# Optimization experiments

Measured on AMD Instinct MI355X. Metric: run time of the kernel, lower is better.

The kernel has to match this reference:

```python
import jax, jax.numpy as jnp
import numpy as np

B, S, HID = 2, 2048, 4096
NH, NKV, HD = 32, 8, 128
SCALING = HD ** -0.5
Q_SIZE = NH * HD          # 4096
KV_SIZE = NKV * HD        # 1024
GROUPS = NH // NKV        # 4


def setup_inputs() -> dict:
    key = jax.random.key(0)
    ks = jax.random.split(key, 5)
    hidden_states = jax.random.normal(ks[0], (B, S, HID), dtype=jnp.float32)
    # Realistic rotary embeddings: cos/sin of position-dependent angles, HF layout [B, S, HD]
    inv_freq = 1.0 / (10000.0 ** (jnp.arange(0, HD, 2, dtype=jnp.float32) / HD))  # [HD/2]
    pos = jnp.arange(S, dtype=jnp.float32)
    freqs = pos[:, None] * inv_freq[None, :]                 # [S, HD/2]
    emb = jnp.concatenate([freqs, freqs], axis=-1)           # [S, HD]
    cos = jnp.broadcast_to(jnp.cos(emb), (B, S, HD))
    sin = jnp.broadcast_to(jnp.sin(emb), (B, S, HD))
    w_qkv = jax.random.normal(ks[1], (Q_SIZE + 2 * KV_SIZE, HID), dtype=jnp.float32) * (HID ** -0.5)
    w_o = jax.random.normal(ks[2], (HID, Q_SIZE), dtype=jnp.float32) * (Q_SIZE ** -0.5)
    return {"hidden_states": hidden_states, "cos": cos, "sin": sin, "w_qkv": w_qkv, "w_o": w_o}


def _rotate_half(x):
    x1, x2 = jnp.split(x, 2, axis=-1)
    return jnp.concatenate([-x2, x1], axis=-1)


def reference(hidden_states, cos, sin, w_qkv, w_o):
    b, s, _ = hidden_states.shape
    # Fused QKV projection (attention_bias=False for llama)
    qkv = jnp.einsum('bsh,oh->bso', hidden_states, w_qkv)    # [B, S, Q+2KV]
    q = qkv[..., :Q_SIZE].reshape(b, s, NH, HD).transpose(0, 2, 1, 3)                       # [B, NH, S, D]
    k = qkv[..., Q_SIZE:Q_SIZE + KV_SIZE].reshape(b, s, NKV, HD).transpose(0, 2, 1, 3)      # [B, NKV, S, D]
    v = qkv[..., Q_SIZE + KV_SIZE:].reshape(b, s, NKV, HD).transpose(0, 2, 1, 3)            # [B, NKV, S, D]
    # Rotary position embedding (HF apply_rotary_pos_emb, unsqueeze over heads)
    c = cos[:, None, :, :]
    sn = sin[:, None, :, :]
    q = q * c + _rotate_half(q) * sn
    k = k * c + _rotate_half(k) * sn
    # GQA: repeat KV heads across groups
    k = jnp.repeat(k, GROUPS, axis=1)   # [B, NH, S, D]
    v = jnp.repeat(v, GROUPS, axis=1)
    # Causal SDPA
    scores = jnp.einsum('bhqd,bhkd->bhqk', q, k) * SCALING
    causal = jnp.tril(jnp.ones((s, s), dtype=bool))
    scores = jnp.where(causal[None, None], scores, jnp.finfo(scores.dtype).min)
    attn = jax.nn.softmax(scores, axis=-1)
    out = jnp.einsum('bhqk,bhkd->bhqd', attn, v)             # [B, NH, S, D]
    out = out.transpose(0, 2, 1, 3).reshape(b, s, Q_SIZE)    # [B, S, HID]
    return jnp.einsum('bso,ho->bsh', out, w_o)
```

## Files before the change

kernel.cpp:

```cpp
#include <hip/hip_runtime.h>
#include <hip/hip_bf16.h>
#include <cstdint>

#define B_DIM 2
#define S_LEN 2048
#define HID 4096
#define NH 32
#define NKV 8
#define HD 128
#define QSZ (NH * HD)
#define KVSZ (NKV * HD)
#define QKVW (QSZ + 2 * KVSZ)
#define SCALING 0.08838834764831845f

typedef __bf16 bf16;
typedef __bf16 bf16x4 __attribute__((ext_vector_type(4)));
typedef __bf16 bf16x8 __attribute__((ext_vector_type(8)));
typedef float floatx4 __attribute__((ext_vector_type(4)));

typedef __attribute__((address_space(1))) void GV;
typedef __attribute__((address_space(3))) void SV;

#define BAR() __builtin_amdgcn_s_barrier()
#define SCHED_FENCE() __builtin_amdgcn_sched_barrier(0)

__global__ __launch_bounds__(256) void cvt3(const float* __restrict__ a, bf16* __restrict__ oa, int na4,
                                            const float* __restrict__ b, bf16* __restrict__ ob, int nb4,
                                            const float* __restrict__ c, bf16* __restrict__ oc, int nc4) {
    int total = na4 + nb4 + nc4;
    int stride = gridDim.x * blockDim.x;
    for (int i = blockIdx.x * blockDim.x + threadIdx.x; i < total; i += stride) {
        const float* src; bf16* dst; int j = i;
        if (j < na4) { src = a; dst = oa; }
        else if ((j -= na4) < nb4) { src = b; dst = ob; }
        else { j -= nb4; src = c; dst = oc; }
        float4 v = ((const float4*)src)[j];
        bf16x4 o;
        o[0] = (bf16)v.x; o[1] = (bf16)v.y; o[2] = (bf16)v.z; o[3] = (bf16)v.w;
        ((bf16x4*)dst)[j] = o;
    }
}

template <int MODE, typename OutT>
__global__ __launch_bounds__(512, 2) void gemm256(const bf16* __restrict__ A,
                                                  const bf16* __restrict__ Bm,
                                                  OutT* __restrict__ C,
                                                  bf16* __restrict__ Qo,
                                                  bf16* __restrict__ Ko,
                                                  bf16* __restrict__ Vo,
                                                  const float* __restrict__ cosp,
                                                  const float* __restrict__ sinp,
                                                  int M, int N, int K) {
    __shared__ __align__(16) char smem[131072];
    (void)M;
    int tiles_n = N >> 8;
    int nwg = gridDim.x;
    int bid = blockIdx.x;
    int wg = (bid & 7) * (nwg >> 3) + (bid >> 3);
    int bm = wg / tiles_n, bn = wg % tiles_n;
    int tid = threadIdx.x;
    int lane = tid & 63, w = tid >> 6;
    int l15 = lane & 15, lg = lane >> 4, l7 = l15 & 7;
    int wm = w >> 2, wn = w & 3;
    const bf16* Ab = A + (size_t)bm * 256 * K;
    const bf16* Bb = Bm + (size_t)bn * 256 * K;

    auto AsP = [&](int buf, int h) -> char* { return smem + (buf * 2 + h) * 16384; };
    auto BsP = [&](int buf, int h) -> char* { return smem + 65536 + (buf * 2 + h) * 16384; };

    int o_lo = tid * 16, o_hi = o_lo + 8192;
    int r_lo = o_lo >> 7, r_hi = o_hi >> 7;
    int eo0 = r_lo * K + ((((o_lo >> 4) & 7) ^ (r_lo & 7)) << 3);
    int eo1 = r_hi * K + ((((o_hi >> 4) & 7) ^ (r_hi & 7)) << 3);
    const bf16* AbH[2] = {Ab, Ab + (size_t)128 * K};
    const bf16* BbH[2] = {Bb, Bb + (size_t)128 * K};

    auto stageA = [&](int buf, int h, int kt) {
        const bf16* base = AbH[h] + kt * 64;
        __builtin_amdgcn_global_load_lds((GV*)(base + eo0), (SV*)(AsP(buf, h) + o_lo), 16, 0, 0);
        __builtin_amdgcn_global_load_lds((GV*)(base + eo1), (SV*)(AsP(buf, h) + o_hi), 16, 0, 0);
    };
    auto stageB = [&](int buf, int h, int kt) {
        const bf16* base = BbH[h] + kt * 64;
        __builtin_amdgcn_global_load_lds((GV*)(base + eo0), (SV*)(BsP(buf, h) + o_lo), 16, 0, 0);
        __builtin_amdgcn_global_load_lds((GV*)(base + eo1), (SV*)(BsP(buf, h) + o_hi), 16, 0, 0);
    };
    auto rdA = [&](int buf, int fr, int kk) -> bf16x8 {
        int off = (fr * 16 + l15) * 128 + ((((kk << 2) | lg) ^ l7) << 4);
        return *(const bf16x8*)(AsP(buf, wm) + off);
    };
    auto rdB = [&](int buf, int fc, int kk) -> bf16x8 {
        int off = ((wn & 1) * 64 + fc * 16 + l15) * 128 + ((((kk << 2) | lg) ^ l7) << 4);
        return *(const bf16x8*)(BsP(buf, wn >> 1) + off);
    };

    floatx4 acc[8][4] = {};
    bf16x8 aF[4][2], bF[4][2];
    int nk = K >> 6, niter = nk >> 1;

    stageA(0, 0, 0); stageA(0, 1, 0); stageB(0, 0, 0); stageB(0, 1, 0);
    stageB(1, 0, 1); stageB(1, 1, 1);
    asm volatile("s_waitcnt vmcnt(4)" ::: "memory");
    SCHED_FENCE();
    BAR();

    auto quad = [&](int ra, int ca) {
        __builtin_amdgcn_s_setprio(1);
#pragma unroll
        for (int fr = 0; fr < 4; ++fr)
#pragma unroll
            for (int fc = 0; fc < 2; ++fc)
#pragma unroll
                for (int kk = 0; kk < 2; ++kk)
                    acc[ra * 4 + fr][ca * 2 + fc] = __builtin_amdgcn_mfma_f32_16x16x32_bf16(
                        aF[fr][kk], bF[ca * 2 + fc][kk], acc[ra * 4 + fr][ca * 2 + fc], 0, 0, 0);
        __builtin_amdgcn_s_setprio(0);
    };

    for (int i = 0; i < niter; ++i) {
        bool nl = (i + 1 < niter);
        int kt1 = 2 * i + 1, kt2 = 2 * i + 2, kt3 = 2 * i + 3;
#pragma unroll
        for (int fr = 0; fr < 4; ++fr)
#pragma unroll
            for (int kk = 0; kk < 2; ++kk) aF[fr][kk] = rdA(0, fr, kk);
#pragma unroll
        for (int fc = 0; fc < 2; ++fc)
#pragma unroll
            for (int kk = 0; kk < 2; ++kk) bF[fc][kk] = rdB(0, fc, kk);
        stageA(1, 0, kt1);
        BAR(); quad(0, 0); BAR();
#pragma unroll
        for (int fc = 2; fc < 4; ++fc)
#pragma unroll
            for (int kk = 0; kk < 2; ++kk) bF[fc][kk] = rdB(0, fc, kk);
        stageA(1, 1, kt1);
        BAR(); quad(0, 1); BAR();
#pragma unroll
        for (int fr = 0; fr < 4; ++fr)
#pragma unroll
            for (int kk = 0; kk < 2; ++kk) aF[fr][kk] = rdA(0, 4 + fr, kk);
        if (nl) stageB(0, 0, kt2);
        BAR(); quad(1, 0); BAR();
        if (nl) stageB(0, 1, kt2);
        BAR(); quad(1, 1);
        if (nl) asm volatile("s_waitcnt vmcnt(4)" ::: "memory");
        else    asm volatile("s_waitcnt vmcnt(0)" ::: "memory");
        SCHED_FENCE();
        BAR();
#pragma unroll
        for (int fr = 0; fr < 4; ++fr)
#pragma unroll
            for (int kk = 0; kk < 2; ++kk) aF[fr][kk] = rdA(1, fr, kk);
#pragma unroll
        for (int fc = 0; fc < 2; ++fc)
#pragma unroll
            for (int kk = 0; kk < 2; ++kk) bF[fc][kk] = rdB(1, fc, kk);
        if (nl) stageA(0, 0, kt2);
        BAR(); quad(0, 0); BAR();
#pragma unroll
        for (int fc = 2; fc < 4; ++fc)
#pragma unroll
            for (int kk = 0; kk < 2; ++kk) bF[fc][kk] = rdB(1, fc, kk);
        if (nl) stageA(0, 1, kt2);
        BAR(); quad(0, 1); BAR();
#pragma unroll
        for (int fr = 0; fr < 4; ++fr)
#pragma unroll
            for (int kk = 0; kk < 2; ++kk) aF[fr][kk] = rdA(1, 4 + fr, kk);
        if (nl) stageB(1, 0, kt3);
        BAR(); quad(1, 0); BAR();
        if (nl) stageB(1, 1, kt3);
        BAR(); quad(1, 1);
        asm volatile("s_waitcnt vmcnt(4)" ::: "memory");
        SCHED_FENCE();
        BAR();
    }

    if constexpr (MODE == 0) {
        int brow = bm * 256 + wm * 128, bcol = bn * 256 + wn * 64;
#pragma unroll
        for (int fr = 0; fr < 8; ++fr)
#pragma unroll
            for (int fc = 0; fc < 4; ++fc) {
                int col = bcol + fc * 16 + l15;
#pragma unroll
                for (int r = 0; r < 4; ++r) {
                    int row = brow + fr * 16 + lg * 4 + r;
                    C[(size_t)row * N + col] = (OutT)acc[fr][fc][r];
                }
            }
    } else {
        __syncthreads();
        int b = (bm * 256) >> 11, s0 = (bm * 256) & (S_LEN - 1);
        int colb = wn * 64, rowb = wm * 128;
        if (bn < 20) {
            bf16* Cb = (bf16*)smem;
#pragma unroll
            for (int fr = 0; fr < 8; ++fr)
#pragma unroll
                for (int fc = 0; fc < 4; ++fc) {
                    int col = colb + fc * 16 + l15;
                    int br = rowb + fr * 16 + lg * 4;
#pragma unroll
                    for (int r = 0; r < 4; ++r) {
                        int row = br + r;
                        Cb[row * 256 + ((((col >> 3) ^ (row & 7)) << 3) | (col & 7))] =
                            (bf16)acc[fr][fc][r];
                    }
                }
            __syncthreads();
            bool isQ = (bn < 16);
            int hh = w & 1;
            int c = l15, d0 = c * 8;
            float scale = isQ ? SCALING : 1.0f;
            float sgn = (c < 8) ? -1.0f : 1.0f;
            bf16* Ob = isQ ? (Qo + ((size_t)(b * NH + bn * 2 + hh) * S_LEN) * HD)
                           : (Ko + ((size_t)(b * NKV + (bn - 16) * 2 + hh) * S_LEN) * HD);
            int slot_s = hh * 16 + c, slot_p = hh * 16 + (c ^ 8);
#pragma unroll
            for (int rd = 0; rd < 16; ++rd) {
                int row = (w >> 1) * 64 + rd * 4 + lg;
                int s = s0 + row;
                bf16x8 xs = *(const bf16x8*)(Cb + row * 256 + ((slot_s ^ (row & 7)) << 3));
                bf16x8 xp = *(const bf16x8*)(Cb + row * 256 + ((slot_p ^ (row & 7)) << 3));
                const float* cr = cosp + ((size_t)b * S_LEN + s) * HD + d0;
                const float* sr = sinp + ((size_t)b * S_LEN + s) * HD + d0;
                float4 c0 = *(const float4*)cr, c1 = *(const float4*)(cr + 4);
                float4 s0v = *(const float4*)sr, s1v = *(const float4*)(sr + 4);
                float cv[8] = {c0.x, c0.y, c0.z, c0.w, c1.x, c1.y, c1.z, c1.w};
                float sv[8] = {s0v.x, s0v.y, s0v.z, s0v.w, s1v.x, s1v.y, s1v.z, s1v.w};
                bf16x8 o;
#pragma unroll
                for (int e = 0; e < 8; ++e)
                    o[e] = (bf16)(((float)xs[e] * cv[e] + sgn * (float)xp[e] * sv[e]) * scale);
                *(bf16x8*)(Ob + (size_t)s * HD + d0) = o;
            }
        } else {
#pragma unroll
            for (int fr = 0; fr < 8; ++fr)
#pragma unroll
                for (int fc = 0; fc < 4; ++fc) {
                    int col = colb + fc * 16 + l15;
                    int br = rowb + fr * 16 + lg * 4;
#pragma unroll
                    for (int r = 0; r < 4; ++r) {
                        int row = br + r;
                        *(bf16*)(smem + col * 512 +
                                 (((((row >> 3) ^ (col & 7)) << 4) | ((row & 7) << 1)))) =
                            (bf16)acc[fr][fc][r];
                    }
                }
            __syncthreads();
            int kvb = (bn - 20) * 2;
            int sc = tid & 31;
            int dgr = tid >> 5;
#pragma unroll
            for (int j = 0; j < 16; ++j) {
                int col = dgr * 16 + j;
                int kv = kvb + (col >> 7), d = col & 127;
                bf16x8 o = *(const bf16x8*)(smem + col * 512 + ((sc ^ (col & 7)) << 4));
                *(bf16x8*)(Vo + ((size_t)(b * NKV + kv) * HD + d) * S_LEN + s0 + sc * 8) = o;
            }
        }
    }
}

__global__ __launch_bounds__(256, 2) void attn_fwd(const bf16* __restrict__ Q,
                                                   const bf16* __restrict__ K,
                                                   const bf16* __restrict__ Vt,
                                                   bf16* __restrict__ O) {
    __shared__ __align__(16) bf16 Ks[2][64 * 128];
    __shared__ __align__(16) bf16 Vs[2][128 * 64];
    __shared__ __align__(16) bf16 Ps[4][32 * 64];

    int ord = blockIdx.x;
    int qt = 15 - (ord >> 6);
    int bh = ord & 63;
    int h = bh & 31, b = bh >> 5;
    int kvh = h >> 2;
    int tid = threadIdx.x, lane = tid & 63, w = tid >> 6;
    int l15 = lane & 15, lg = lane >> 4, l7 = l15 & 7, lg4 = lg * 4;
    int q0 = qt * 128;
    int qbw = q0 + w * 32;

    const bf16* Qb = Q + ((size_t)(b * NH + h) * S_LEN) * HD;
    const bf16* Kb = K + ((size_t)(b * NKV + kvh) * S_LEN) * HD;
    const bf16* Vb = Vt + ((size_t)(b * NKV + kvh) * HD) * S_LEN;

    bf16x8 qf[2][4];
#pragma unroll
    for (int i = 0; i < 2; ++i)
#pragma unroll
        for (int ks = 0; ks < 4; ++ks)
            qf[i][ks] = *(const bf16x8*)(Qb + (size_t)(qbw + i * 16 + l15) * HD + ks * 32 + lg * 8);

    floatx4 accO[2][8] = {};
    float m_run[2] = {-1e30f, -1e30f}, l_run[2] = {0.f, 0.f};

    char* Pc = (char*)Ps[w];
    int nt = 2 * qt + 2;

    auto stageK = [&](int buf, int t) {
        int kv0 = t * 64;
#pragma unroll
        for (int it = 0; it < 4; ++it) {
            int o = it * 4096 + tid * 16;
            int r = o >> 8, pb = (o >> 4) & 15;
            int lb = pb ^ (r & 7);
            __builtin_amdgcn_global_load_lds((GV*)(Kb + (size_t)(kv0 + r) * HD + lb * 8),
                                             (SV*)((char*)Ks[buf] + o), 16, 0, 0);
        }
    };
    auto stageV = [&](int buf, int t) {
        int kv0 = t * 64;
#pragma unroll
        for (int it = 0; it < 4; ++it) {
            int o = it * 4096 + tid * 16;
            int d = o >> 7, pb = (o >> 4) & 7;
            int lb = pb ^ (d & 7);
            __builtin_amdgcn_global_load_lds((GV*)(Vb + (size_t)d * S_LEN + kv0 + lb * 8),
                                             (SV*)((char*)Vs[buf] + o), 16, 0, 0);
        }
    };

    stageK(0, 0);
    stageV(0, 0);

    for (int t = 0; t < nt; ++t) {
        int cur = t & 1;
        int kv0 = t * 64;
        bool more = (t + 1 < nt);
        if (more) { stageK(cur ^ 1, t + 1); stageV(cur ^ 1, t + 1); }
        if (more) asm volatile("s_waitcnt vmcnt(8)" ::: "memory");
        else      asm volatile("s_waitcnt vmcnt(0)" ::: "memory");
        SCHED_FENCE();
        BAR();

        const char* Kc = (const char*)Ks[cur];
        const char* Vc = (const char*)Vs[cur];
        floatx4 s[2][4] = {};
        __builtin_amdgcn_s_setprio(1);
#pragma unroll
        for (int nm = 0; nm < 4; ++nm)
#pragma unroll
            for (int ks = 0; ks < 4; ++ks) {
                bf16x8 kf = *(const bf16x8*)(Kc + (nm * 16 + l15) * 256 +
                                             ((((ks << 2) | lg) ^ l7) << 4));
                s[0][nm] = __builtin_amdgcn_mfma_f32_16x16x32_bf16(kf, qf[0][ks], s[0][nm], 0, 0, 0);
                s[1][nm] = __builtin_amdgcn_mfma_f32_16x16x32_bf16(kf, qf[1][ks], s[1][nm], 0, 0, 0);
            }
        __builtin_amdgcn_s_setprio(0);

#pragma unroll
        for (int i = 0; i < 2; ++i) {
            if (kv0 + 63 > qbw + i * 16) {
                int qg = qbw + i * 16 + l15;
#pragma unroll
                for (int nm = 0; nm < 4; ++nm)
#pragma unroll
                    for (int r = 0; r < 4; ++r)
                        if (kv0 + nm * 16 + lg4 + r > qg) s[i][nm][r] = -1e30f;
            }
            float t0 = fmaxf(fmaxf(s[i][0][0], s[i][0][1]), fmaxf(s[i][0][2], s[i][0][3]));
            float t1 = fmaxf(fmaxf(s[i][1][0], s[i][1][1]), fmaxf(s[i][1][2], s[i][1][3]));
            float t2 = fmaxf(fmaxf(s[i][2][0], s[i][2][1]), fmaxf(s[i][2][2], s[i][2][3]));
            float t3 = fmaxf(fmaxf(s[i][3][0], s[i][3][1]), fmaxf(s[i][3][2], s[i][3][3]));
            float pm = fmaxf(fmaxf(t0, t1), fmaxf(t2, t3));
            pm = fmaxf(pm, __shfl_xor(pm, 16));
            pm = fmaxf(pm, __shfl_xor(pm, 32));
            bool need = !__all(pm - m_run[i] <= 8.f);
            float corr = 1.f;
            if (need) {
                float mn = fmaxf(m_run[i], pm);
                corr = __expf(m_run[i] - mn);
                m_run[i] = mn;
            }
            float mn = m_run[i];
            float sum = 0.f;
#pragma unroll
            for (int nm = 0; nm < 4; ++nm) {
                bf16x4 pk;
#pragma unroll
                for (int r = 0; r < 4; ++r) {
                    float p = __expf(s[i][nm][r] - mn);
                    sum += p;
                    pk[r] = (bf16)p;
                }
                *(bf16x4*)(Pc + (i * 16 + l15) * 128 +
                           ((((nm << 1) | (lg >> 1)) ^ l7) << 4) + ((lg & 1) << 3)) = pk;
            }
            sum += __shfl_xor(sum, 16);
            sum += __shfl_xor(sum, 32);
            if (need) {
                l_run[i] = l_run[i] * corr + sum;
#pragma unroll
                for (int r = 0; r < 4; ++r) {
                    float cr = __shfl(corr, lg4 + r);
#pragma unroll
                    for (int g = 0; g < 8; ++g) accO[i][g][r] *= cr;
                }
            } else {
                l_run[i] += sum;
            }
        }

        asm volatile("s_waitcnt lgkmcnt(0)" ::: "memory");
        SCHED_FENCE();

        bf16x8 pf[2][2];
#pragma unroll
        for (int i = 0; i < 2; ++i)
#pragma unroll
            for (int ks = 0; ks < 2; ++ks)
                pf[i][ks] = *(const bf16x8*)(Pc + (i * 16 + l15) * 128 +
                                             ((((ks << 2) | lg) ^ l7) << 4));
        __builtin_amdgcn_s_setprio(1);
#pragma unroll
        for (int g = 0; g < 8; ++g)
#pragma unroll
            for (int ks = 0; ks < 2; ++ks) {
                bf16x8 vf = *(const bf16x8*)(Vc + (g * 16 + l15) * 128 +
                                             ((((ks << 2) | lg) ^ l7) << 4));
                accO[0][g] = __builtin_amdgcn_mfma_f32_16x16x32_bf16(pf[0][ks], vf, accO[0][g], 0, 0, 0);
                accO[1][g] = __builtin_amdgcn_mfma_f32_16x16x32_bf16(pf[1][ks], vf, accO[1][g], 0, 0, 0);
            }
        __builtin_amdgcn_s_setprio(0);
        BAR();
    }

#pragma unroll
    for (int i = 0; i < 2; ++i) {
        float inv = 1.f / l_run[i];
#pragma unroll
        for (int r = 0; r < 4; ++r) {
            float vinv = __shfl(inv, lg4 + r);
            int qg = qbw + i * 16 + lg4 + r;
            size_t ob = ((size_t)(b * S_LEN + qg) * NH + h) * HD;
#pragma unroll
            for (int g = 0; g < 8; ++g)
                O[ob + g * 16 + l15] = (bf16)(accO[i][g][r] * vinv);
        }
    }
}

extern "C" void kernel_launch(void* const* d_in, const int* in_sizes, int n_in,
                              void* d_out, int out_size, void* d_ws, size_t ws_size,
                              hipStream_t stream) {
    const float* hs   = (const float*)d_in[0];
    const float* cosp = (const float*)d_in[1];
    const float* sinp = (const float*)d_in[2];
    const float* wqkv = (const float*)d_in[3];
    const float* wo   = (const float*)d_in[4];
    float* out = (float*)d_out;

    char* ws = (char*)d_ws;
    size_t off = 0;
    auto alloc = [&](size_t bytes) {
        char* p = ws + off;
        off += (bytes + 255) & ~(size_t)255;
        return p;
    };
    const size_t n_hs = (size_t)B_DIM * S_LEN * HID;
    const size_t n_wqkv = (size_t)QKVW * HID;
    const size_t n_wo = (size_t)HID * QSZ;

    bf16* hs_b   = (bf16*)alloc(n_hs * 2);
    bf16* wqkv_b = (bf16*)alloc(n_wqkv * 2);
    bf16* wo_b   = (bf16*)alloc(n_wo * 2);
    bf16* Qb  = (bf16*)alloc((size_t)B_DIM * NH * S_LEN * HD * 2);
    bf16* Kb  = (bf16*)alloc((size_t)B_DIM * NKV * S_LEN * HD * 2);
    bf16* Vtb = (bf16*)alloc((size_t)B_DIM * NKV * HD * S_LEN * 2);
    bf16* attn_b = hs_b;

    cvt3<<<2048, 256, 0, stream>>>(hs, hs_b, (int)(n_hs >> 2),
                                   wqkv, wqkv_b, (int)(n_wqkv >> 2),
                                   wo, wo_b, (int)(n_wo >> 2));

    gemm256<1, bf16><<<(4096 / 256) * (6144 / 256), 512, 0, stream>>>(
        hs_b, wqkv_b, (bf16*)nullptr, Qb, Kb, Vtb, cosp, sinp, B_DIM * S_LEN, QKVW, HID);

    attn_fwd<<<B_DIM * NH * (S_LEN / 128), 256, 0, stream>>>(Qb, Kb, Vtb, attn_b);

    gemm256<0, float><<<(4096 / 256) * (4096 / 256), 512, 0, stream>>>(
        attn_b, wo_b, out, nullptr, nullptr, nullptr, nullptr, nullptr,
        B_DIM * S_LEN, HID, HID);
}
```

Baseline: 481.0 us.

## Overlap w_o bf16 conversion with QKV GEMM using extra workgroups

The w_o fp32-to-bf16 conversion moves out of the standalone conversion kernel and into 64 extra workgroups appended to the QKV GEMM launch. Those blocks run a grid-stride convert loop while the GEMM tiles compute, so the memory-bound conversion can overlap with compute-bound work. The grid swizzle now uses the GEMM block count instead of gridDim. The risk is that the extra blocks compete for CUs and bandwidth, and the GEMM's tail or dispatch order may change.

```diff
diff --git a/kernel.cpp b/kernel.cpp
--- a/kernel.cpp
+++ b/kernel.cpp
@@ -24,16 +24,14 @@
 #define BAR() __builtin_amdgcn_s_barrier()
 #define SCHED_FENCE() __builtin_amdgcn_sched_barrier(0)
 
-__global__ __launch_bounds__(256) void cvt3(const float* __restrict__ a, bf16* __restrict__ oa, int na4,
-                                            const float* __restrict__ b, bf16* __restrict__ ob, int nb4,
-                                            const float* __restrict__ c, bf16* __restrict__ oc, int nc4) {
-    int total = na4 + nb4 + nc4;
+__global__ __launch_bounds__(256) void cvt2(const float* __restrict__ a, bf16* __restrict__ oa, int na4,
+                                            const float* __restrict__ b, bf16* __restrict__ ob, int nb4) {
+    int total = na4 + nb4;
     int stride = gridDim.x * blockDim.x;
     for (int i = blockIdx.x * blockDim.x + threadIdx.x; i < total; i += stride) {
         const float* src; bf16* dst; int j = i;
         if (j < na4) { src = a; dst = oa; }
-        else if ((j -= na4) < nb4) { src = b; dst = ob; }
-        else { j -= nb4; src = c; dst = oc; }
+        else { j -= na4; src = b; dst = ob; }
         float4 v = ((const float4*)src)[j];
         bf16x4 o;
         o[0] = (bf16)v.x; o[1] = (bf16)v.y; o[2] = (bf16)v.z; o[3] = (bf16)v.w;
@@ -50,15 +48,27 @@
                                                   bf16* __restrict__ Vo,
                                                   const float* __restrict__ cosp,
                                                   const float* __restrict__ sinp,
+                                                  const float* __restrict__ cvt_src,
+                                                  bf16* __restrict__ cvt_dst,
+                                                  int cvt_n4, int ngemm,
                                                   int M, int N, int K) {
     __shared__ __align__(16) char smem[131072];
     (void)M;
+    int bid = blockIdx.x;
+    int tid = threadIdx.x;
+    if (bid >= ngemm) {
+        int stride = (gridDim.x - ngemm) * 512;
+        for (int i = (bid - ngemm) * 512 + tid; i < cvt_n4; i += stride) {
+            float4 v = ((const float4*)cvt_src)[i];
+            bf16x4 o;
+            o[0] = (bf16)v.x; o[1] = (bf16)v.y; o[2] = (bf16)v.z; o[3] = (bf16)v.w;
+            ((bf16x4*)cvt_dst)[i] = o;
+        }
+        return;
+    }
     int tiles_n = N >> 8;
-    int nwg = gridDim.x;
-    int bid = blockIdx.x;
-    int wg = (bid & 7) * (nwg >> 3) + (bid >> 3);
+    int wg = (bid & 7) * (ngemm >> 3) + (bid >> 3);
     int bm = wg / tiles_n, bn = wg % tiles_n;
-    int tid = threadIdx.x;
     int lane = tid & 63, w = tid >> 6;
     int l15 = lane & 15, lg = lane >> 4, l7 = l15 & 7;
     int wm = w >> 2, wn = w & 3;
@@ -473,16 +483,18 @@
     bf16* Vtb = (bf16*)alloc((size_t)B_DIM * NKV * HD * S_LEN * 2);
     bf16* attn_b = hs_b;
 
-    cvt3<<<2048, 256, 0, stream>>>(hs, hs_b, (int)(n_hs >> 2),
-                                   wqkv, wqkv_b, (int)(n_wqkv >> 2),
-                                   wo, wo_b, (int)(n_wo >> 2));
-
-    gemm256<1, bf16><<<(4096 / 256) * (6144 / 256), 512, 0, stream>>>(
-        hs_b, wqkv_b, (bf16*)nullptr, Qb, Kb, Vtb, cosp, sinp, B_DIM * S_LEN, QKVW, HID);
+    cvt2<<<1536, 256, 0, stream>>>(hs, hs_b, (int)(n_hs >> 2),
+                                   wqkv, wqkv_b, (int)(n_wqkv >> 2));
+
+    const int ngemm1 = (4096 / 256) * (6144 / 256);
+    gemm256<1, bf16><<<ngemm1 + 64, 512, 0, stream>>>(
+        hs_b, wqkv_b, (bf16*)nullptr, Qb, Kb, Vtb, cosp, sinp,
+        wo, wo_b, (int)(n_wo >> 2), ngemm1, B_DIM * S_LEN, QKVW, HID);
 
     attn_fwd<<<B_DIM * NH * (S_LEN / 128), 256, 0, stream>>>(Qb, Kb, Vtb, attn_b);
 
     gemm256<0, float><<<(4096 / 256) * (4096 / 256), 512, 0, stream>>>(
         attn_b, wo_b, out, nullptr, nullptr, nullptr, nullptr, nullptr,
+        nullptr, nullptr, 0, (4096 / 256) * (4096 / 256),
         B_DIM * S_LEN, HID, HID);
 }
```

Result: faster. 469.6 us, median of 2 (-2.4%).
